# Kernel tuning notes

Hardware: AMD Instinct MI355X
Metric: run time of the kernel (lower is better)

Reference implementation:

```python
import jax, jax.numpy as jnp
import numpy as np

EPS = 1e-3  # Keras LayerNormalization default epsilon


def setup_inputs() -> dict:
    key = jax.random.key(0)
    ks = jax.random.split(key, 10)
    B, S, D, U = 4, 4096, 1024, 1024
    sc_in = 1.0 / np.sqrt(D)
    sc_u = 1.0 / np.sqrt(U)
    return {
        "inputs": jax.random.normal(ks[0], (B, S, D), dtype=jnp.float32),
        "w1": jax.random.normal(ks[1], (D, U), dtype=jnp.float32) * sc_in,
        "b1": jnp.zeros((U,), dtype=jnp.float32),
        "w2": jax.random.normal(ks[2], (U, U), dtype=jnp.float32) * sc_u,
        "b2": jnp.zeros((U,), dtype=jnp.float32),
        "wg": jax.random.normal(ks[3], (D, U), dtype=jnp.float32) * sc_in,
        "bg": jnp.zeros((U,), dtype=jnp.float32),
        "ws": jax.random.normal(ks[4], (D, U), dtype=jnp.float32) * sc_in,
        "bs": jnp.zeros((U,), dtype=jnp.float32),
        "gamma": jnp.ones((U,), dtype=jnp.float32),
        "beta": jnp.zeros((U,), dtype=jnp.float32),
    }


def reference(inputs, w1, b1, w2, b2, wg, bg, ws, bs, gamma, beta):
    # hidden branch: Dense(relu) -> (dropout inactive at inference) -> Dense
    h = jax.nn.relu(jnp.einsum('bsd,du->bsu', inputs, w1) + b1)
    x = jnp.einsum('bsu,uv->bsv', h, w2) + b2
    # gate on raw inputs
    g = jax.nn.sigmoid(jnp.einsum('bsd,du->bsu', inputs, wg) + bg)
    # skip projection
    s = jnp.einsum('bsd,du->bsu', inputs, ws) + bs
    y = x * g + s
    # LayerNormalization over last axis (Keras default eps=1e-3)
    mu = jnp.mean(y, axis=-1, keepdims=True)
    var = jnp.mean(jnp.square(y - mu), axis=-1, keepdims=True)
    return (y - mu) * jax.lax.rsqrt(var + EPS) * gamma + beta
```

## Files before the change

### kernel.cpp

```cpp
#include <hip/hip_runtime.h>
#include <hip/hip_bf16.h>

typedef short short8 __attribute__((ext_vector_type(8)));
typedef float f32x4 __attribute__((ext_vector_type(4)));

#define M_TOT 16384
#define NDIM  1024
#define BK 32
#define NT (NDIM / BK)

static __device__ __forceinline__ unsigned short f2bf(float f) {
  unsigned int u = __builtin_bit_cast(unsigned int, f);
  unsigned int r = (u + 0x7fffu + ((u >> 16) & 1u)) >> 16;
  return (unsigned short)r;
}
static __device__ __forceinline__ float bf2f(unsigned short u) {
  return __builtin_bit_cast(float, ((unsigned int)u) << 16);
}

#define CLB() asm volatile("" ::: "memory")
#define VMW(N) asm volatile("s_waitcnt vmcnt(" #N ")" ::: "memory")
#define BAR() do { CLB(); __builtin_amdgcn_s_barrier(); CLB(); } while (0)

__global__ __launch_bounds__(256) void cast_in(const float* __restrict__ in,
                                               unsigned short* __restrict__ out,
                                               int n4) {
  int i = blockIdx.x * 256 + threadIdx.x;
  if (i >= n4) return;
  float4 v = reinterpret_cast<const float4*>(in)[i];
  ushort4 o;
  o.x = f2bf(v.x); o.y = f2bf(v.y); o.z = f2bf(v.z); o.w = f2bf(v.w);
  reinterpret_cast<ushort4*>(out)[i] = o;
}

__global__ __launch_bounds__(256) void tcast(const float* __restrict__ src,
                                             unsigned short* __restrict__ dst) {
  __shared__ unsigned short tile[32][33];
  int bx = blockIdx.x * 32, by = blockIdx.y * 32;
  int x = threadIdx.x & 31, y = threadIdx.x >> 5;
#pragma unroll
  for (int i = 0; i < 32; i += 8)
    tile[y + i][x] = f2bf(src[(size_t)(by + y + i) * NDIM + bx + x]);
  __syncthreads();
#pragma unroll
  for (int i = 0; i < 32; i += 8)
    dst[(size_t)(bx + y + i) * NDIM + by + x] = tile[x][y + i];
}

__global__ __launch_bounds__(256, 2) void trigemm(
    const unsigned short* __restrict__ A,
    const unsigned short* __restrict__ W1t,
    const unsigned short* __restrict__ Wgt,
    const unsigned short* __restrict__ Wst,
    const float* __restrict__ b1,
    const float* __restrict__ bg,
    const float* __restrict__ bs,
    unsigned short* __restrict__ H,
    unsigned short* __restrict__ G,
    unsigned short* __restrict__ S) {
  __shared__ __align__(16) unsigned short lds[2][4][128][BK];

  const int tid = threadIdx.x;
  const int lane = tid & 63;
  const int wave = tid >> 6;
  const int wm = wave >> 1;
  const int wn = wave & 1;

  const int id = blockIdx.x;
  const int xcd = id & 7;
  const int slot = id >> 3;
  const int rblk = xcd + 8 * (slot >> 3);
  const int cblk = slot & 7;
  const int m0 = rblk * 128, n0 = cblk * 128;

  const unsigned short* gA = A + (size_t)m0 * NDIM;
  const unsigned short* gW[3] = {W1t + (size_t)n0 * NDIM, Wgt + (size_t)n0 * NDIM,
                                 Wst + (size_t)n0 * NDIM};

  f32x4 acc[3][4][4] = {};

  auto stage = [&](int buf, int kt) {
#pragma unroll
    for (int q = 0; q < 8; ++q) {
      const int mat = q >> 1;
      int local = (q & 1) * 256 + tid;
      int row = local >> 2;
      int c = (local & 3) ^ ((row >> 1) & 3);
      const unsigned short* g =
          (mat == 0 ? gA : gW[mat - 1]) + (size_t)row * NDIM + kt * BK + c * 8;
      unsigned short* l = &lds[buf][0][0][0] +
                          (size_t)(q * 256 + (tid & ~63)) * 8;
      __builtin_amdgcn_global_load_lds(
          (__attribute__((address_space(1))) void*)g,
          (__attribute__((address_space(3))) void*)l, 16, 0, 0);
    }
  };

  auto compute = [&](int buf) {
    short8 af[4];
#pragma unroll
    for (int mi = 0; mi < 4; ++mi) {
      int row = wm * 64 + mi * 16 + (lane & 15);
      int cs = (lane >> 4) ^ ((row >> 1) & 3);
      af[mi] = *reinterpret_cast<const short8*>(&lds[buf][0][row][cs * 8]);
    }
#pragma unroll
    for (int w = 0; w < 3; ++w) {
      short8 bf[4];
#pragma unroll
      for (int nj = 0; nj < 4; ++nj) {
        int row = wn * 64 + nj * 16 + (lane & 15);
        int cs = (lane >> 4) ^ ((row >> 1) & 3);
        bf[nj] = *reinterpret_cast<const short8*>(&lds[buf][1 + w][row][cs * 8]);
      }
      __builtin_amdgcn_s_setprio(1);
#pragma unroll
      for (int mi = 0; mi < 4; ++mi)
#pragma unroll
        for (int nj = 0; nj < 4; ++nj)
          acc[w][mi][nj] = __builtin_amdgcn_mfma_f32_16x16x32_bf16(
              af[mi], bf[nj], acc[w][mi][nj], 0, 0, 0);
      __builtin_amdgcn_s_setprio(0);
    }
  };

  stage(0, 0);
  for (int t = 0; t < NT; ++t) {
    const int cur = t & 1;
    if (t + 1 < NT) {
      stage(cur ^ 1, t + 1);
      VMW(8);
    } else {
      VMW(0);
    }
    BAR();
    compute(cur);
    BAR();
  }

  const int crow0 = m0 + wm * 64;
  const int ccol0 = n0 + wn * 64;
#pragma unroll
  for (int w = 0; w < 3; ++w) {
    const float* bptr = (w == 0) ? b1 : (w == 1) ? bg : bs;
    unsigned short* optr = (w == 0) ? H : (w == 1) ? G : S;
#pragma unroll
    for (int mi = 0; mi < 4; ++mi) {
#pragma unroll
      for (int nj = 0; nj < 4; ++nj) {
        int row = crow0 + mi * 16 + ((lane >> 4) << 2);
        int col = ccol0 + nj * 16 + (lane & 15);
        float bc = bptr[col];
#pragma unroll
        for (int r = 0; r < 4; ++r) {
          float v = acc[w][mi][nj][r] + bc;
          if (w == 0) v = fmaxf(v, 0.f);
          else if (w == 1) v = 1.f / (1.f + __expf(-v));
          optr[(size_t)(row + r) * NDIM + col] = f2bf(v);
        }
      }
    }
  }
}

__global__ __launch_bounds__(512, 2) void gemm_y(
    const unsigned short* __restrict__ A,
    const unsigned short* __restrict__ Bt,
    const float* __restrict__ bias,
    unsigned short* __restrict__ O,
    const unsigned short* __restrict__ G,
    const unsigned short* __restrict__ S) {
  __shared__ __align__(16) unsigned short lds[4][2][256][BK];

  const int tid = threadIdx.x;
  const int lane = tid & 63;
  const int wave = tid >> 6;
  const int wm = wave >> 2;
  const int wn = wave & 3;

  const int id = blockIdx.x;
  const int xcd = id & 7;
  const int slot0 = id >> 3;
  const int rblk = xcd + 8 * (slot0 >> 2);
  const int cblk = slot0 & 3;
  const int m0 = rblk * 256, n0 = cblk * 256;

  const unsigned short* gA = A + (size_t)m0 * NDIM;
  const unsigned short* gB = Bt + (size_t)n0 * NDIM;

  f32x4 acc[8][4] = {};

  auto stage = [&](int slot, int kt) {
#pragma unroll
    for (int q = 0; q < 4; ++q) {
      int cid = q * 512 + tid;
      int mat = q >> 1;
      int local = cid & 1023;
      int row = local >> 2;
      int c = (local & 3) ^ ((row >> 1) & 3);
      const unsigned short* g =
          (mat ? gB : gA) + (size_t)row * NDIM + kt * BK + c * 8;
      unsigned short* l = &lds[slot][mat][0][0] +
                          (size_t)((q * 512 + (tid & ~63)) & 1023) * 8;
      __builtin_amdgcn_global_load_lds(
          (__attribute__((address_space(1))) void*)g,
          (__attribute__((address_space(3))) void*)l, 16, 0, 0);
    }
  };

  auto compute = [&](int slot) {
    short8 af[8], bf[4];
#pragma unroll
    for (int nj = 0; nj < 4; ++nj) {
      int row = wn * 64 + nj * 16 + (lane & 15);
      int cs = (lane >> 4) ^ ((row >> 1) & 3);
      bf[nj] = *reinterpret_cast<const short8*>(&lds[slot][1][row][cs * 8]);
    }
#pragma unroll
    for (int mi = 0; mi < 8; ++mi) {
      int row = wm * 128 + mi * 16 + (lane & 15);
      int cs = (lane >> 4) ^ ((row >> 1) & 3);
      af[mi] = *reinterpret_cast<const short8*>(&lds[slot][0][row][cs * 8]);
    }
    __builtin_amdgcn_s_setprio(1);
#pragma unroll
    for (int mi = 0; mi < 8; ++mi)
#pragma unroll
      for (int nj = 0; nj < 4; ++nj)
        acc[mi][nj] = __builtin_amdgcn_mfma_f32_16x16x32_bf16(
            af[mi], bf[nj], acc[mi][nj], 0, 0, 0);
    __builtin_amdgcn_s_setprio(0);
  };

  stage(0, 0);
  stage(1, 1);
  stage(2, 2);
  VMW(8);
  BAR();

#pragma unroll 4
  for (int t = 0; t < NT - 4; ++t) {
    stage((t + 3) & 3, t + 3);
    compute(t & 3);
    VMW(8);
    BAR();
  }
  stage(3, 31);
  compute(0);
  VMW(8);
  BAR();
  compute(1);
  VMW(4);
  BAR();
  compute(2);
  VMW(0);
  BAR();
  compute(3);

  const int crow0 = m0 + wm * 128;
  const int ccol0 = n0 + wn * 64;
#pragma unroll
  for (int mi = 0; mi < 8; ++mi) {
#pragma unroll
    for (int nj = 0; nj < 4; ++nj) {
      int row = crow0 + mi * 16 + ((lane >> 4) << 2);
      int col = ccol0 + nj * 16 + (lane & 15);
      float bc = bias[col];
#pragma unroll
      for (int r = 0; r < 4; ++r) {
        float v = acc[mi][nj][r] + bc;
        size_t idx = (size_t)(row + r) * NDIM + col;
        O[idx] = f2bf(v * bf2f(G[idx]) + bf2f(S[idx]));
      }
    }
  }
}

__global__ __launch_bounds__(256) void layernorm_bf(
    const unsigned short* __restrict__ Ybf, float* __restrict__ Out,
    const float* __restrict__ gamma, const float* __restrict__ beta) {
  const int tid = threadIdx.x;
  const unsigned short* y = Ybf + (size_t)blockIdx.x * NDIM;
  ushort4 u = reinterpret_cast<const ushort4*>(y)[tid];
  float v0 = bf2f(u.x), v1 = bf2f(u.y), v2 = bf2f(u.z), v3 = bf2f(u.w);
  float s1 = v0 + v1 + v2 + v3;
  float s2 = v0 * v0 + v1 * v1 + v2 * v2 + v3 * v3;
#pragma unroll
  for (int o = 32; o > 0; o >>= 1) {
    s1 += __shfl_down(s1, o, 64);
    s2 += __shfl_down(s2, o, 64);
  }
  __shared__ float red[8];
  int wave = tid >> 6, lane = tid & 63;
  if (lane == 0) { red[wave] = s1; red[wave + 4] = s2; }
  __syncthreads();
  float S1 = red[0] + red[1] + red[2] + red[3];
  float S2 = red[4] + red[5] + red[6] + red[7];
  float mu = S1 * (1.f / NDIM);
  float var = S2 * (1.f / NDIM) - mu * mu;
  float inv = rsqrtf(var + 1e-3f);
  float4 gm = reinterpret_cast<const float4*>(gamma)[tid];
  float4 bt = reinterpret_cast<const float4*>(beta)[tid];
  float4 o;
  o.x = (v0 - mu) * inv * gm.x + bt.x;
  o.y = (v1 - mu) * inv * gm.y + bt.y;
  o.z = (v2 - mu) * inv * gm.z + bt.z;
  o.w = (v3 - mu) * inv * gm.w + bt.w;
  reinterpret_cast<float4*>(Out + (size_t)blockIdx.x * NDIM)[tid] = o;
}

extern "C" void kernel_launch(void* const* d_in, const int* in_sizes, int n_in,
                              void* d_out, int out_size, void* d_ws, size_t ws_size,
                              hipStream_t stream) {
  const float* inp = (const float*)d_in[0];
  const float* w1 = (const float*)d_in[1];
  const float* b1 = (const float*)d_in[2];
  const float* w2 = (const float*)d_in[3];
  const float* b2 = (const float*)d_in[4];
  const float* wg = (const float*)d_in[5];
  const float* bg = (const float*)d_in[6];
  const float* wsk = (const float*)d_in[7];
  const float* bs = (const float*)d_in[8];
  const float* gamma = (const float*)d_in[9];
  const float* beta = (const float*)d_in[10];

  char* p = (char*)d_ws;
  const size_t act_bf16 = (size_t)M_TOT * NDIM * 2;
  const size_t w_bf16 = (size_t)NDIM * NDIM * 2;
  unsigned short* Ain = (unsigned short*)p; p += act_bf16;
  unsigned short* H   = (unsigned short*)p; p += act_bf16;
  unsigned short* G   = (unsigned short*)p; p += act_bf16;
  unsigned short* S   = (unsigned short*)p; p += act_bf16;
  unsigned short* Ybf = (unsigned short*)p; p += act_bf16;
  unsigned short* W1t = (unsigned short*)p; p += w_bf16;
  unsigned short* W2t = (unsigned short*)p; p += w_bf16;
  unsigned short* Wgt = (unsigned short*)p; p += w_bf16;
  unsigned short* Wst = (unsigned short*)p; p += w_bf16;

  cast_in<<<(M_TOT * NDIM / 4 + 255) / 256, 256, 0, stream>>>(inp, Ain, M_TOT * NDIM / 4);
  dim3 tg(32, 32);
  tcast<<<tg, 256, 0, stream>>>(w1, W1t);
  tcast<<<tg, 256, 0, stream>>>(w2, W2t);
  tcast<<<tg, 256, 0, stream>>>(wg, Wgt);
  tcast<<<tg, 256, 0, stream>>>(wsk, Wst);

  trigemm<<<(M_TOT / 128) * (NDIM / 128), 256, 0, stream>>>(
      Ain, W1t, Wgt, Wst, b1, bg, bs, H, G, S);
  gemm_y<<<(M_TOT / 256) * (NDIM / 256), 512, 0, stream>>>(H, W2t, b2, Ybf, G, S);
  layernorm_bf<<<M_TOT, 256, 0, stream>>>(Ybf, (float*)d_out, gamma, beta);
}
```

Before: 195.2 us.

## Fuse LayerNorm into second GEMM with full-row tiles and merge weight casts

Replaces the LDS-pipelined 256x256 second GEMM and the separate LayerNorm kernel with one kernel. Each block owns 64 full rows and computes bias, gate and skip plus row statistics in registers, reducing them with shuffles and shared memory. This removes the bf16 intermediate Y round trip, one launch, and the bf16 rounding of Y. The trade-off is that the GEMM now loads operands straight from global into double-buffered registers without LDS sharing, which adds redundant cache traffic and register pressure. The four weight transpose-cast launches are also merged into one 3D-grid launch.

```diff
diff --git a/kernel.cpp b/kernel.cpp
--- a/kernel.cpp
+++ b/kernel.cpp
@@ -33,8 +33,14 @@
   reinterpret_cast<ushort4*>(out)[i] = o;
 }
 
-__global__ __launch_bounds__(256) void tcast(const float* __restrict__ src,
-                                             unsigned short* __restrict__ dst) {
+__global__ __launch_bounds__(256) void tcast4(
+    const float* __restrict__ w1, const float* __restrict__ w2,
+    const float* __restrict__ wg, const float* __restrict__ ws,
+    unsigned short* __restrict__ W1t, unsigned short* __restrict__ W2t,
+    unsigned short* __restrict__ Wgt, unsigned short* __restrict__ Wst) {
+  const int z = blockIdx.z;
+  const float* src = (z == 0) ? w1 : (z == 1) ? w2 : (z == 2) ? wg : ws;
+  unsigned short* dst = (z == 0) ? W1t : (z == 1) ? W2t : (z == 2) ? Wgt : Wst;
   __shared__ unsigned short tile[32][33];
   int bx = blockIdx.x * 32, by = blockIdx.y * 32;
   int x = threadIdx.x & 31, y = threadIdx.x >> 5;
@@ -163,150 +169,132 @@
   }
 }
 
-__global__ __launch_bounds__(512, 2) void gemm_y(
-    const unsigned short* __restrict__ A,
-    const unsigned short* __restrict__ Bt,
-    const float* __restrict__ bias,
-    unsigned short* __restrict__ O,
+__global__ __launch_bounds__(512, 2) void gemm_y_ln(
+    const unsigned short* __restrict__ H,
+    const unsigned short* __restrict__ W2t,
+    const float* __restrict__ b2,
     const unsigned short* __restrict__ G,
-    const unsigned short* __restrict__ S) {
-  __shared__ __align__(16) unsigned short lds[4][2][256][BK];
-
+    const unsigned short* __restrict__ S,
+    const float* __restrict__ gamma,
+    const float* __restrict__ beta,
+    float* __restrict__ Out) {
   const int tid = threadIdx.x;
   const int lane = tid & 63;
   const int wave = tid >> 6;
-  const int wm = wave >> 2;
-  const int wn = wave & 3;
-
-  const int id = blockIdx.x;
-  const int xcd = id & 7;
-  const int slot0 = id >> 3;
-  const int rblk = xcd + 8 * (slot0 >> 2);
-  const int cblk = slot0 & 3;
-  const int m0 = rblk * 256, n0 = cblk * 256;
-
-  const unsigned short* gA = A + (size_t)m0 * NDIM;
-  const unsigned short* gB = Bt + (size_t)n0 * NDIM;
-
-  f32x4 acc[8][4] = {};
-
-  auto stage = [&](int slot, int kt) {
-#pragma unroll
-    for (int q = 0; q < 4; ++q) {
-      int cid = q * 512 + tid;
-      int mat = q >> 1;
-      int local = cid & 1023;
-      int row = local >> 2;
-      int c = (local & 3) ^ ((row >> 1) & 3);
-      const unsigned short* g =
-          (mat ? gB : gA) + (size_t)row * NDIM + kt * BK + c * 8;
-      unsigned short* l = &lds[slot][mat][0][0] +
-                          (size_t)((q * 512 + (tid & ~63)) & 1023) * 8;
-      __builtin_amdgcn_global_load_lds(
-          (__attribute__((address_space(1))) void*)g,
-          (__attribute__((address_space(3))) void*)l, 16, 0, 0);
-    }
-  };
-
-  auto compute = [&](int slot) {
-    short8 af[8], bf[4];
-#pragma unroll
-    for (int nj = 0; nj < 4; ++nj) {
-      int row = wn * 64 + nj * 16 + (lane & 15);
-      int cs = (lane >> 4) ^ ((row >> 1) & 3);
-      bf[nj] = *reinterpret_cast<const short8*>(&lds[slot][1][row][cs * 8]);
-    }
-#pragma unroll
-    for (int mi = 0; mi < 8; ++mi) {
-      int row = wm * 128 + mi * 16 + (lane & 15);
-      int cs = (lane >> 4) ^ ((row >> 1) & 3);
-      af[mi] = *reinterpret_cast<const short8*>(&lds[slot][0][row][cs * 8]);
-    }
-    __builtin_amdgcn_s_setprio(1);
-#pragma unroll
-    for (int mi = 0; mi < 8; ++mi)
-#pragma unroll
-      for (int nj = 0; nj < 4; ++nj)
+  const int m0 = blockIdx.x * 64;
+  const int c0 = wave * 128;
+  const int lr = lane & 15;
+  const int lk = lane >> 4;
+
+  const unsigned short* aBase = H + (size_t)(m0 + lr) * NDIM + lk * 8;
+  const unsigned short* bBase = W2t + (size_t)(c0 + lr) * NDIM + lk * 8;
+
+  f32x4 acc[4][8] = {};
+  short8 aA[4], bA[8], aB[4], bB[8];
+
+  auto loadA = [&](short8* d, int kt) {
+#pragma unroll
+    for (int mi = 0; mi < 4; ++mi)
+      d[mi] = *reinterpret_cast<const short8*>(aBase + (size_t)mi * 16 * NDIM + kt * BK);
+  };
+  auto loadB = [&](short8* d, int kt) {
+#pragma unroll
+    for (int nj = 0; nj < 8; ++nj)
+      d[nj] = *reinterpret_cast<const short8*>(bBase + (size_t)nj * 16 * NDIM + kt * BK);
+  };
+  auto mfmaAll = [&](short8* a, short8* b) {
+#pragma unroll
+    for (int mi = 0; mi < 4; ++mi)
+#pragma unroll
+      for (int nj = 0; nj < 8; ++nj)
         acc[mi][nj] = __builtin_amdgcn_mfma_f32_16x16x32_bf16(
-            af[mi], bf[nj], acc[mi][nj], 0, 0, 0);
-    __builtin_amdgcn_s_setprio(0);
-  };
-
-  stage(0, 0);
-  stage(1, 1);
-  stage(2, 2);
-  VMW(8);
-  BAR();
-
-#pragma unroll 4
-  for (int t = 0; t < NT - 4; ++t) {
-    stage((t + 3) & 3, t + 3);
-    compute(t & 3);
-    VMW(8);
-    BAR();
-  }
-  stage(3, 31);
-  compute(0);
-  VMW(8);
-  BAR();
-  compute(1);
-  VMW(4);
-  BAR();
-  compute(2);
-  VMW(0);
-  BAR();
-  compute(3);
-
-  const int crow0 = m0 + wm * 128;
-  const int ccol0 = n0 + wn * 64;
-#pragma unroll
-  for (int mi = 0; mi < 8; ++mi) {
-#pragma unroll
-    for (int nj = 0; nj < 4; ++nj) {
-      int row = crow0 + mi * 16 + ((lane >> 4) << 2);
-      int col = ccol0 + nj * 16 + (lane & 15);
-      float bc = bias[col];
+            a[mi], b[nj], acc[mi][nj], 0, 0, 0);
+  };
+
+  loadA(aA, 0); loadB(bA, 0);
+  for (int t = 0; t < NT; t += 2) {
+    loadA(aB, t + 1); loadB(bB, t + 1);
+    mfmaAll(aA, bA);
+    if (t + 2 < NT) { loadA(aA, t + 2); loadB(bA, t + 2); }
+    mfmaAll(aB, bB);
+  }
+
+  float bcol[8], gmc[8], btc[8];
+#pragma unroll
+  for (int nj = 0; nj < 8; ++nj) {
+    int col = c0 + nj * 16 + lr;
+    bcol[nj] = b2[col];
+    gmc[nj] = gamma[col];
+    btc[nj] = beta[col];
+  }
+
+  float s1[4][4], s2[4][4];
+#pragma unroll
+  for (int mi = 0; mi < 4; ++mi) {
+#pragma unroll
+    for (int r = 0; r < 4; ++r) {
+      int row = m0 + mi * 16 + lk * 4 + r;
+      float rs1 = 0.f, rs2 = 0.f;
+#pragma unroll
+      for (int nj = 0; nj < 8; ++nj) {
+        int col = c0 + nj * 16 + lr;
+        size_t idx = (size_t)row * NDIM + col;
+        float v = acc[mi][nj][r] + bcol[nj];
+        v = v * bf2f(G[idx]) + bf2f(S[idx]);
+        acc[mi][nj][r] = v;
+        rs1 += v; rs2 += v * v;
+      }
+      s1[mi][r] = rs1; s2[mi][r] = rs2;
+    }
+  }
+
+#pragma unroll
+  for (int off = 1; off < 16; off <<= 1) {
+#pragma unroll
+    for (int mi = 0; mi < 4; ++mi)
 #pragma unroll
       for (int r = 0; r < 4; ++r) {
-        float v = acc[mi][nj][r] + bc;
-        size_t idx = (size_t)(row + r) * NDIM + col;
-        O[idx] = f2bf(v * bf2f(G[idx]) + bf2f(S[idx]));
-      }
-    }
-  }
-}
-
-__global__ __launch_bounds__(256) void layernorm_bf(
-    const unsigned short* __restrict__ Ybf, float* __restrict__ Out,
-    const float* __restrict__ gamma, const float* __restrict__ beta) {
-  const int tid = threadIdx.x;
-  const unsigned short* y = Ybf + (size_t)blockIdx.x * NDIM;
-  ushort4 u = reinterpret_cast<const ushort4*>(y)[tid];
-  float v0 = bf2f(u.x), v1 = bf2f(u.y), v2 = bf2f(u.z), v3 = bf2f(u.w);
-  float s1 = v0 + v1 + v2 + v3;
-  float s2 = v0 * v0 + v1 * v1 + v2 * v2 + v3 * v3;
-#pragma unroll
-  for (int o = 32; o > 0; o >>= 1) {
-    s1 += __shfl_down(s1, o, 64);
-    s2 += __shfl_down(s2, o, 64);
-  }
-  __shared__ float red[8];
-  int wave = tid >> 6, lane = tid & 63;
-  if (lane == 0) { red[wave] = s1; red[wave + 4] = s2; }
+        s1[mi][r] += __shfl_xor(s1[mi][r], off, 16);
+        s2[mi][r] += __shfl_xor(s2[mi][r], off, 16);
+      }
+  }
+
+  __shared__ float redS[8][64];
+  __shared__ float redQ[8][64];
+  __shared__ float2 fin[64];
+#pragma unroll
+  for (int kk = 0; kk < 16; ++kk) {
+    if ((lane & 15) == kk) {
+      int rl = (kk >> 2) * 16 + lk * 4 + (kk & 3);
+      redS[wave][rl] = s1[kk >> 2][kk & 3];
+      redQ[wave][rl] = s2[kk >> 2][kk & 3];
+    }
+  }
   __syncthreads();
-  float S1 = red[0] + red[1] + red[2] + red[3];
-  float S2 = red[4] + red[5] + red[6] + red[7];
-  float mu = S1 * (1.f / NDIM);
-  float var = S2 * (1.f / NDIM) - mu * mu;
-  float inv = rsqrtf(var + 1e-3f);
-  float4 gm = reinterpret_cast<const float4*>(gamma)[tid];
-  float4 bt = reinterpret_cast<const float4*>(beta)[tid];
-  float4 o;
-  o.x = (v0 - mu) * inv * gm.x + bt.x;
-  o.y = (v1 - mu) * inv * gm.y + bt.y;
-  o.z = (v2 - mu) * inv * gm.z + bt.z;
-  o.w = (v3 - mu) * inv * gm.w + bt.w;
-  reinterpret_cast<float4*>(Out + (size_t)blockIdx.x * NDIM)[tid] = o;
+  if (tid < 64) {
+    float a1 = 0.f, a2 = 0.f;
+#pragma unroll
+    for (int w = 0; w < 8; ++w) { a1 += redS[w][tid]; a2 += redQ[w][tid]; }
+    float mu = a1 * (1.f / NDIM);
+    float var = a2 * (1.f / NDIM) - mu * mu;
+    fin[tid] = make_float2(mu, rsqrtf(var + 1e-3f));
+  }
+  __syncthreads();
+
+#pragma unroll
+  for (int mi = 0; mi < 4; ++mi) {
+#pragma unroll
+    for (int r = 0; r < 4; ++r) {
+      int rl = mi * 16 + lk * 4 + r;
+      float2 f = fin[rl];
+      float* orow = Out + (size_t)(m0 + rl) * NDIM;
+#pragma unroll
+      for (int nj = 0; nj < 8; ++nj) {
+        int col = c0 + nj * 16 + lr;
+        orow[col] = (acc[mi][nj][r] - f.x) * f.y * gmc[nj] + btc[nj];
+      }
+    }
+  }
 }
 
 extern "C" void kernel_launch(void* const* d_in, const int* in_sizes, int n_in,
@@ -331,21 +319,16 @@
   unsigned short* H   = (unsigned short*)p; p += act_bf16;
   unsigned short* G   = (unsigned short*)p; p += act_bf16;
   unsigned short* S   = (unsigned short*)p; p += act_bf16;
-  unsigned short* Ybf = (unsigned short*)p; p += act_bf16;
   unsigned short* W1t = (unsigned short*)p; p += w_bf16;
   unsigned short* W2t = (unsigned short*)p; p += w_bf16;
   unsigned short* Wgt = (unsigned short*)p; p += w_bf16;
   unsigned short* Wst = (unsigned short*)p; p += w_bf16;
 
   cast_in<<<(M_TOT * NDIM / 4 + 255) / 256, 256, 0, stream>>>(inp, Ain, M_TOT * NDIM / 4);
-  dim3 tg(32, 32);
-  tcast<<<tg, 256, 0, stream>>>(w1, W1t);
-  tcast<<<tg, 256, 0, stream>>>(w2, W2t);
-  tcast<<<tg, 256, 0, stream>>>(wg, Wgt);
-  tcast<<<tg, 256, 0, stream>>>(wsk, Wst);
+  tcast4<<<dim3(32, 32, 4), 256, 0, stream>>>(w1, w2, wg, wsk, W1t, W2t, Wgt, Wst);
 
   trigemm<<<(M_TOT / 128) * (NDIM / 128), 256, 0, stream>>>(
       Ain, W1t, Wgt, Wst, b1, bg, bs, H, G, S);
-  gemm_y<<<(M_TOT / 256) * (NDIM / 256), 512, 0, stream>>>(H, W2t, b2, Ybf, G, S);
-  layernorm_bf<<<M_TOT, 256, 0, stream>>>(Ybf, (float*)d_out, gamma, beta);
-}
+  gemm_y_ln<<<M_TOT / 64, 512, 0, stream>>>(H, W2t, b2, G, S, gamma, beta,
+                                            (float*)d_out);
+}
```

Measured after the change: 257.5 us. 31.9% more time.

## Enlarge trigemm tile to 256 rows with 512 threads and merge weight transposes

Applied to the files above, without the earlier changes.

The fused triple GEMM now uses a 256x128 output tile with 8 waves per block, so each staged weight tile is reused across twice as many input rows. The LDS layout is flattened and staging is rewritten to match, with the wait count adjusted to 5 loads per stage. The four weight transpose-cast launches are merged into one grid-z launch to cut launch overhead. The cost is that launch bounds of 512 threads with 2 blocks per CU likely cap registers near 128 per thread, while each thread still holds 192 accumulator floats. That risks register spills and lower achieved occupancy.

```diff
diff --git a/kernel.cpp b/kernel.cpp
--- a/kernel.cpp
+++ b/kernel.cpp
@@ -33,8 +33,14 @@
   reinterpret_cast<ushort4*>(out)[i] = o;
 }
 
-__global__ __launch_bounds__(256) void tcast(const float* __restrict__ src,
-                                             unsigned short* __restrict__ dst) {
+__global__ __launch_bounds__(256) void tcast4(
+    const float* __restrict__ w1, const float* __restrict__ w2,
+    const float* __restrict__ wg, const float* __restrict__ ws,
+    unsigned short* __restrict__ W1t, unsigned short* __restrict__ W2t,
+    unsigned short* __restrict__ Wgt, unsigned short* __restrict__ Wst) {
+  const int z = blockIdx.z;
+  const float* src = (z == 0) ? w1 : (z == 1) ? w2 : (z == 2) ? wg : ws;
+  unsigned short* dst = (z == 0) ? W1t : (z == 1) ? W2t : (z == 2) ? Wgt : Wst;
   __shared__ unsigned short tile[32][33];
   int bx = blockIdx.x * 32, by = blockIdx.y * 32;
   int x = threadIdx.x & 31, y = threadIdx.x >> 5;
@@ -47,7 +53,7 @@
     dst[(size_t)(bx + y + i) * NDIM + by + x] = tile[x][y + i];
 }
 
-__global__ __launch_bounds__(256, 2) void trigemm(
+__global__ __launch_bounds__(512, 2) void trigemm(
     const unsigned short* __restrict__ A,
     const unsigned short* __restrict__ W1t,
     const unsigned short* __restrict__ Wgt,
@@ -58,20 +64,22 @@
     unsigned short* __restrict__ H,
     unsigned short* __restrict__ G,
     unsigned short* __restrict__ S) {
-  __shared__ __align__(16) unsigned short lds[2][4][128][BK];
+  __shared__ __align__(16) unsigned short lds[2][20480];
 
   const int tid = threadIdx.x;
   const int lane = tid & 63;
   const int wave = tid >> 6;
   const int wm = wave >> 1;
   const int wn = wave & 1;
+  const int lr = lane & 15;
+  const int lk = lane >> 4;
 
   const int id = blockIdx.x;
   const int xcd = id & 7;
   const int slot = id >> 3;
   const int rblk = xcd + 8 * (slot >> 3);
   const int cblk = slot & 7;
-  const int m0 = rblk * 128, n0 = cblk * 128;
+  const int m0 = rblk * 256, n0 = cblk * 128;
 
   const unsigned short* gA = A + (size_t)m0 * NDIM;
   const unsigned short* gW[3] = {W1t + (size_t)n0 * NDIM, Wgt + (size_t)n0 * NDIM,
@@ -81,15 +89,23 @@
 
   auto stage = [&](int buf, int kt) {
 #pragma unroll
-    for (int q = 0; q < 8; ++q) {
-      const int mat = q >> 1;
-      int local = (q & 1) * 256 + tid;
-      int row = local >> 2;
-      int c = (local & 3) ^ ((row >> 1) & 3);
-      const unsigned short* g =
-          (mat == 0 ? gA : gW[mat - 1]) + (size_t)row * NDIM + kt * BK + c * 8;
-      unsigned short* l = &lds[buf][0][0][0] +
-                          (size_t)(q * 256 + (tid & ~63)) * 8;
+    for (int q = 0; q < 5; ++q) {
+      int cid = q * 512 + tid;
+      const unsigned short* g;
+      if (q < 2) {
+        int row = cid >> 2;
+        int c = (cid & 3) ^ ((row >> 1) & 3);
+        g = gA + (size_t)row * NDIM + kt * BK + c * 8;
+      } else {
+        int local = cid - 1024 - (q - 2) * 512 + (q - 2) * 512;
+        local = cid - 1024;
+        int w = q - 2;
+        int lrow = local & 511;
+        int row = lrow >> 2;
+        int c = (lrow & 3) ^ ((row >> 1) & 3);
+        g = gW[w] + (size_t)row * NDIM + kt * BK + c * 8;
+      }
+      unsigned short* l = &lds[buf][0] + (size_t)(q * 512 + (tid & ~63)) * 8;
       __builtin_amdgcn_global_load_lds(
           (__attribute__((address_space(1))) void*)g,
           (__attribute__((address_space(3))) void*)l, 16, 0, 0);
@@ -100,18 +116,19 @@
     short8 af[4];
 #pragma unroll
     for (int mi = 0; mi < 4; ++mi) {
-      int row = wm * 64 + mi * 16 + (lane & 15);
-      int cs = (lane >> 4) ^ ((row >> 1) & 3);
-      af[mi] = *reinterpret_cast<const short8*>(&lds[buf][0][row][cs * 8]);
+      int row = wm * 64 + mi * 16 + lr;
+      int cs = lk ^ ((row >> 1) & 3);
+      af[mi] = *reinterpret_cast<const short8*>(&lds[buf][row * 32 + cs * 8]);
     }
 #pragma unroll
     for (int w = 0; w < 3; ++w) {
       short8 bf[4];
 #pragma unroll
       for (int nj = 0; nj < 4; ++nj) {
-        int row = wn * 64 + nj * 16 + (lane & 15);
-        int cs = (lane >> 4) ^ ((row >> 1) & 3);
-        bf[nj] = *reinterpret_cast<const short8*>(&lds[buf][1 + w][row][cs * 8]);
+        int row = wn * 64 + nj * 16 + lr;
+        int cs = lk ^ ((row >> 1) & 3);
+        bf[nj] = *reinterpret_cast<const short8*>(
+            &lds[buf][8192 + w * 4096 + row * 32 + cs * 8]);
       }
       __builtin_amdgcn_s_setprio(1);
 #pragma unroll
@@ -129,7 +146,7 @@
     const int cur = t & 1;
     if (t + 1 < NT) {
       stage(cur ^ 1, t + 1);
-      VMW(8);
+      VMW(5);
     } else {
       VMW(0);
     }
@@ -148,8 +165,8 @@
     for (int mi = 0; mi < 4; ++mi) {
 #pragma unroll
       for (int nj = 0; nj < 4; ++nj) {
-        int row = crow0 + mi * 16 + ((lane >> 4) << 2);
-        int col = ccol0 + nj * 16 + (lane & 15);
+        int row = crow0 + mi * 16 + (lk << 2);
+        int col = ccol0 + nj * 16 + lr;
         float bc = bptr[col];
 #pragma unroll
         for (int r = 0; r < 4; ++r) {
@@ -338,13 +355,9 @@
   unsigned short* Wst = (unsigned short*)p; p += w_bf16;
 
   cast_in<<<(M_TOT * NDIM / 4 + 255) / 256, 256, 0, stream>>>(inp, Ain, M_TOT * NDIM / 4);
-  dim3 tg(32, 32);
-  tcast<<<tg, 256, 0, stream>>>(w1, W1t);
-  tcast<<<tg, 256, 0, stream>>>(w2, W2t);
-  tcast<<<tg, 256, 0, stream>>>(wg, Wgt);
-  tcast<<<tg, 256, 0, stream>>>(wsk, Wst);
-
-  trigemm<<<(M_TOT / 128) * (NDIM / 128), 256, 0, stream>>>(
+  tcast4<<<dim3(32, 32, 4), 256, 0, stream>>>(w1, w2, wg, wsk, W1t, W2t, Wgt, Wst);
+
+  trigemm<<<(M_TOT / 256) * (NDIM / 128), 512, 0, stream>>>(
       Ain, W1t, Wgt, Wst, b1, bg, bs, H, G, S);
   gemm_y<<<(M_TOT / 256) * (NDIM / 256), 512, 0, stream>>>(H, W2t, b2, Ybf, G, S);
   layernorm_bf<<<M_TOT, 256, 0, stream>>>(Ybf, (float*)d_out, gamma, beta);
```

New measurement: 189.2 us. -3.1%, faster.
